# Performance work log

Measured on AMD Instinct MI355X. Metric: run time of the kernel, lower is better.

## Reference

```python
import jax, jax.numpy as jnp
import numpy as np


def setup_inputs() -> dict:
    key = jax.random.key(0)
    k1, k2 = jax.random.split(key)
    B, D, N = 4096, 3072, 50000  # chunk size, flattened CIFAR image dim, dataset size
    x = jax.random.normal(k1, (B, D), dtype=jnp.float32)
    y = jax.random.normal(k2, (B, D), dtype=jnp.float32)
    # buffers: initialized to +inf-like large value / zeros as in the torch module
    min_dists = jnp.full((N,), 1e9, dtype=jnp.float32)
    nn_indices = jnp.zeros((N,), dtype=jnp.int32)
    return {
        "x": x,
        "y": y,
        "min_dists": min_dists,
        "nn_indices": nn_indices,
        "x_idx_start": 1024,
        "y_idx_start": 4096,
    }


def reference(x, y, min_dists, nn_indices, x_idx_start, y_idx_start):
    # K == 1, cosine_dist == False path of KNNComputerNoCheck.forward
    B = x.shape[0]
    xf = x.reshape(B, -1)
    yf = y.reshape(y.shape[0], -1)
    # pairwise euclidean distances (same math as torch.cdist p=2)
    x2 = jnp.sum(xf * xf, axis=1, keepdims=True)        # [B,1]
    y2 = jnp.sum(yf * yf, axis=1)                        # [B]
    d2 = x2 + y2[None, :] - 2.0 * (xf @ yf.T)            # [B,B]
    dist = jnp.sqrt(jnp.maximum(d2, 0.0))
    new_min = jnp.min(dist, axis=1)                      # [B]
    nn = jnp.argmin(dist, axis=1).astype(nn_indices.dtype)
    # buffer scatter-update: min with existing slice, unconditional index overwrite
    old = jax.lax.dynamic_slice(min_dists, (x_idx_start,), (B,))
    min_dists = jax.lax.dynamic_update_slice(
        min_dists, jnp.minimum(new_min, old), (x_idx_start,))
    nn_indices = jax.lax.dynamic_update_slice(
        nn_indices, nn + jnp.int32(y_idx_start), (x_idx_start,))
    return min_dists, nn_indices
```

## Files before the change

### kernel.cpp

```cpp
#include <hip/hip_runtime.h>
#include <math.h>

#define BSZ 4096
#define DDIM 3072
#define QBM 256
#define QBN 256
#define QBK 64
#define NBUF 4
#define NT   (DDIM / QBK)
#define BM 128
#define BN 128
#define BK 32
#define LDK 40
#define S_Q 20.0f
#define DELTA 32.0f
#define NSLOT 16

typedef _Float16 half8 __attribute__((ext_vector_type(8)));
typedef float    floatx4 __attribute__((ext_vector_type(4)));
typedef int      intx4  __attribute__((ext_vector_type(4)));
typedef unsigned char u8;

__device__ __forceinline__ unsigned long long pack_key(float t, unsigned int j) {
    unsigned int b = __float_as_uint(t);
    b = (b & 0x80000000u) ? ~b : (b | 0x80000000u);
    return ((unsigned long long)b << 32) | (unsigned long long)j;
}

__device__ __forceinline__ float unpack_val(unsigned long long key) {
    unsigned int ub = (unsigned int)(key >> 32);
    unsigned int b = (ub & 0x80000000u) ? (ub ^ 0x80000000u) : ~ub;
    return __uint_as_float(b);
}

__device__ __forceinline__ void split_f16(float v, _Float16& hi, _Float16& lo) {
    hi = (_Float16)v;
    lo = (_Float16)(v - (float)hi);
}

__device__ __forceinline__ void gll16(const void* g, void* l) {
    __builtin_amdgcn_global_load_lds(
        (const __attribute__((address_space(1))) void*)g,
        (__attribute__((address_space(3))) void*)l,
        16, 0, 0);
}

__global__ __launch_bounds__(256)
void split_norms_kernel(const float* __restrict__ x, const float* __restrict__ y,
                        const float* __restrict__ mind_in, const int* __restrict__ nn_in,
                        const int* __restrict__ xs_p,
                        u8* __restrict__ A8, u8* __restrict__ B8,
                        float* __restrict__ x2, float* __restrict__ y2,
                        float* __restrict__ out_mind, float* __restrict__ out_nn,
                        int N) {
    {
        const int xs = *xs_p;
        const int n = blockIdx.x * 256 + threadIdx.x;
        if (n < N) {
            const int i = n - xs;
            if (i < 0 || i >= BSZ) {
                out_mind[n] = mind_in[n];
                out_nn[n]   = (float)nn_in[n];
            }
        }
    }

    const int lane = threadIdx.x & 63;
    const int row  = blockIdx.x * 4 + (threadIdx.x >> 6);
    const bool isx = row < BSZ;
    const int r = isx ? row : row - BSZ;
    const float* src = (isx ? x : y) + (size_t)r * DDIM;
    unsigned int* dst = (unsigned int*)((isx ? A8 : B8) + (size_t)r * DDIM);

    float s = 0.f;
    #pragma unroll
    for (int it = 0; it < 12; ++it) {
        float4 v = *(const float4*)(src + it * 256 + lane * 4);
        float fv[4] = {v.x, v.y, v.z, v.w};
        union { signed char b[4]; unsigned int u; } q;
        #pragma unroll
        for (int i = 0; i < 4; i++) {
            s += fv[i] * fv[i];
            int qi = __float2int_rn(fv[i] * S_Q);
            qi = (qi > 127) ? 127 : ((qi < -127) ? -127 : qi);
            q.b[i] = (signed char)qi;
        }
        dst[it * 64 + lane] = q.u;
    }
    #pragma unroll
    for (int off = 32; off > 0; off >>= 1) s += __shfl_down(s, off, 64);
    if (lane == 0) { if (isx) x2[r] = s; else y2[r] = s; }
}

__global__ __launch_bounds__(512, 1)
void gemm_i8_kernel(const u8* __restrict__ A8, const u8* __restrict__ B8,
                    const float* __restrict__ y2, _Float16* __restrict__ Dt) {
    extern __shared__ u8 smem[];
    u8* const sA = smem;
    u8* const sB = smem + NBUF * QBM * QBK;

    const int tid = threadIdx.x;
    const int bid = blockIdx.x;
    const int sw  = ((bid & 7) << 5) | (bid >> 3);
    const int row0 = (sw >> 4) * QBM;
    const int col0 = (sw & 15) * QBN;

    const int wid    = tid >> 6;
    const int lane   = tid & 63;
    const int wave_m = wid >> 2;
    const int wave_n = wid & 3;
    const int lrow   = lane & 15;
    const int quad   = lane >> 4;

    intx4 acc[8][4];
    #pragma unroll
    for (int m = 0; m < 8; m++)
        #pragma unroll
        for (int n = 0; n < 4; n++) acc[m][n] = (intx4){0, 0, 0, 0};

    const int rg = lane >> 2, cg = lane & 3;
    const int g  = cg ^ ((rg >> 1) & 3);
    const int wr = (wid & 3) * 64;
    const u8* stSrc = ((wid < 4) ? (A8 + (size_t)row0 * DDIM)
                                 : (B8 + (size_t)col0 * DDIM))
                      + (size_t)(wr + rg) * DDIM + g * 16;
    u8* stDst = ((wid < 4) ? sA : sB) + wr * QBK + lane * 16;

    const int coff = (quad ^ ((lrow >> 1) & 3)) * 16;

#define STAGE(T)                                                              \
    do {                                                                      \
        const u8* p_ = stSrc + (size_t)(T) * QBK;                             \
        u8* d_ = stDst + ((T) & 3) * (QBM * QBK);                             \
        _Pragma("unroll")                                                     \
        for (int it_ = 0; it_ < 4; ++it_)                                     \
            gll16(p_ + (size_t)16 * it_ * DDIM, d_ + it_ * 16 * QBK);         \
    } while (0)

#define READF(FA, FB, T)                                                      \
    do {                                                                      \
        const u8* bA_ = sA + ((T) & 3) * (QBM * QBK);                         \
        const u8* bB_ = sB + ((T) & 3) * (QBN * QBK);                         \
        _Pragma("unroll")                                                     \
        for (int m = 0; m < 8; m++)                                           \
            FA[m] = *(const intx4*)&bA_[(wave_m * 128 + m * 16 + lrow) * QBK + coff]; \
        _Pragma("unroll")                                                     \
        for (int n = 0; n < 4; n++)                                           \
            FB[n] = *(const intx4*)&bB_[(wave_n * 64 + n * 16 + lrow) * QBK + coff]; \
    } while (0)

#define MFMA_ALL(FA, FB)                                                      \
    do {                                                                      \
        __builtin_amdgcn_s_setprio(1);                                        \
        _Pragma("unroll")                                                     \
        for (int m = 0; m < 8; m++)                                           \
            _Pragma("unroll")                                                 \
            for (int n = 0; n < 4; n++)                                       \
                acc[m][n] = __builtin_amdgcn_mfma_i32_16x16x64_i8(            \
                    FA[m], FB[n], acc[m][n], 0, 0, 0);                        \
        __builtin_amdgcn_s_setprio(0);                                        \
    } while (0)

#define GSTEP(T, VM, CFA, CFB, NFA, NFB)                                      \
    do {                                                                      \
        asm volatile("s_waitcnt lgkmcnt(0)" ::: "memory");                    \
        asm volatile("s_waitcnt vmcnt(" VM ")" ::: "memory");                 \
        __builtin_amdgcn_s_barrier();                                         \
        __builtin_amdgcn_sched_barrier(0);                                    \
        if ((T) + 1 < NT) READF(NFA, NFB, (T) + 1);                           \
        if ((T) + 4 < NT) STAGE((T) + 4);                                     \
        MFMA_ALL(CFA, CFB);                                                   \
    } while (0)

    intx4 fa0[8], fb0[4], fa1[8], fb1[4];

    STAGE(0); STAGE(1); STAGE(2); STAGE(3);
    asm volatile("s_waitcnt vmcnt(12)" ::: "memory");
    __builtin_amdgcn_s_barrier();
    __builtin_amdgcn_sched_barrier(0);
    READF(fa0, fb0, 0);

    for (int t = 0; t < NT - 4; t += 2) {
        GSTEP(t,     "8", fa0, fb0, fa1, fb1);
        GSTEP(t + 1, "8", fa1, fb1, fa0, fb0);
    }
    GSTEP(NT - 4, "8", fa0, fb0, fa1, fb1);
    GSTEP(NT - 3, "4", fa1, fb1, fa0, fb0);
    GSTEP(NT - 2, "0", fa0, fb0, fa1, fb1);
    asm volatile("s_waitcnt lgkmcnt(0)" ::: "memory");
    MFMA_ALL(fa1, fb1);
#undef GSTEP
#undef MFMA_ALL
#undef READF
#undef STAGE

    const float inv2 = 2.0f / (S_Q * S_Q);
    float y2v[4];
    int   jv[4];
    #pragma unroll
    for (int n = 0; n < 4; n++) {
        jv[n]  = col0 + wave_n * 64 + n * 16 + lrow;
        y2v[n] = y2[jv[n]] - 3072.0f;
    }
    #pragma unroll
    for (int m = 0; m < 8; m++) {
        #pragma unroll
        for (int reg = 0; reg < 4; reg++) {
            const int i = row0 + wave_m * 128 + m * 16 + quad * 4 + reg;
            #pragma unroll
            for (int n = 0; n < 4; n++) {
                const float t = y2v[n] - inv2 * (float)acc[m][n][reg];
                Dt[(size_t)i * BSZ + jv[n]] = (_Float16)t;
            }
        }
    }
}

__global__ __launch_bounds__(256)
void scan_exact_kernel(const _Float16* __restrict__ Dt,
                       const float* __restrict__ x, const float* __restrict__ y,
                       const float* __restrict__ y2, const float* __restrict__ x2,
                       const float* __restrict__ mind_in,
                       const int* __restrict__ xs_p, const int* __restrict__ ys_p,
                       float* __restrict__ out_mind, float* __restrict__ out_nn) {
    const int lane = threadIdx.x & 63;
    const int wv   = threadIdx.x >> 6;
    const int row  = blockIdx.x * 4 + wv;
    const _Float16* p = Dt + (size_t)row * BSZ;

    __shared__ unsigned int cand[4][NSLOT];
    if (lane < NSLOT) cand[wv][lane] = 0u;

    float m = 1e30f;
    #pragma unroll
    for (int it = 0; it < 8; ++it) {
        half8 v = *(const half8*)(p + it * 512 + lane * 8);
        float lm = fminf(fminf(fminf((float)v[0], (float)v[1]),
                               fminf((float)v[2], (float)v[3])),
                         fminf(fminf((float)v[4], (float)v[5]),
                               fminf((float)v[6], (float)v[7])));
        m = fminf(m, lm);
    }
    #pragma unroll
    for (int off = 32; off > 0; off >>= 1) m = fminf(m, __shfl_xor(m, off, 64));
    const float thr = m + DELTA;

    unsigned int cnt = 0;
    const unsigned long long lanemask = (1ull << lane) - 1ull;
    #pragma unroll
    for (int it = 0; it < 8; ++it) {
        half8 v = *(const half8*)(p + it * 512 + lane * 8);
        #pragma unroll
        for (int j = 0; j < 8; ++j) {
            const bool ok = ((float)v[j] <= thr);
            const unsigned long long mk = __ballot(ok);
            if (ok) {
                const unsigned int pos = cnt + (unsigned int)__popcll(mk & lanemask);
                if (pos < NSLOT) cand[wv][pos] = it * 512 + lane * 8 + j;
            }
            cnt += (unsigned int)__popcll(mk);
        }
    }
    int cnum = (int)((cnt < NSLOT) ? cnt : NSLOT);

    const float* xr = x + (size_t)row * DDIM;
    float bt = 1e30f;
    int   bj = 0x7fffffff;
    for (int c = 0; c < cnum; ++c) {
        const int col = (int)(cand[wv][c] & (BSZ - 1));
        const float* yr = y + (size_t)col * DDIM;
        float s = 0.f;
        #pragma unroll
        for (int k = 0; k < 12; k++) {
            float4 a = *(const float4*)(xr + k * 256 + lane * 4);
            float4 b = *(const float4*)(yr + k * 256 + lane * 4);
            s += a.x * b.x + a.y * b.y + a.z * b.z + a.w * b.w;
        }
        #pragma unroll
        for (int off = 32; off > 0; off >>= 1) s += __shfl_down(s, off, 64);
        s = __shfl(s, 0, 64);
        const float t = y2[col] - 2.0f * s;
        if (t < bt || (t == bt && col < bj)) { bt = t; bj = col; }
    }

    if (lane == 0) {
        const int xs = *xs_p, ys = *ys_p;
        const int n = xs + row;
        const float d = sqrtf(fmaxf(x2[row] + bt, 0.f));
        out_mind[n] = fminf(mind_in[n], d);
        out_nn[n]   = (float)(bj + ys);
    }
}

__global__ __launch_bounds__(256)
void norms_init_kernel(const float* __restrict__ x, const float* __restrict__ y,
                       float* __restrict__ x2, float* __restrict__ y2,
                       unsigned long long* __restrict__ keys) {
    const int row = blockIdx.x;
    const float* p = (row < BSZ) ? (x + (size_t)row * DDIM)
                                 : (y + (size_t)(row - BSZ) * DDIM);
    const float4* p4 = (const float4*)p;
    float s = 0.f;
    for (int k = threadIdx.x; k < DDIM / 4; k += 256) {
        float4 v = p4[k];
        s += v.x * v.x + v.y * v.y + v.z * v.z + v.w * v.w;
    }
    #pragma unroll
    for (int off = 32; off > 0; off >>= 1) s += __shfl_down(s, off, 64);
    __shared__ float ls[4];
    const int lane = threadIdx.x & 63, w = threadIdx.x >> 6;
    if (lane == 0) ls[w] = s;
    __syncthreads();
    if (threadIdx.x == 0) {
        float tot = ls[0] + ls[1] + ls[2] + ls[3];
        if (row < BSZ) { x2[row] = tot; keys[row] = ~0ull; }
        else           { y2[row - BSZ] = tot; }
    }
}

__global__ __launch_bounds__(256, 3)
void gemm_min_kernel(const float* __restrict__ x, const float* __restrict__ y,
                     const float* __restrict__ y2,
                     unsigned long long* __restrict__ keys) {
    __shared__ _Float16 Ahi[BM * LDK];
    __shared__ _Float16 Alo[BM * LDK];
    __shared__ _Float16 Bhi[BN * LDK];
    __shared__ _Float16 Blo[BN * LDK];
    __shared__ unsigned long long rowmin[BM];

    const int tid  = threadIdx.x;
    const int row0 = blockIdx.y * BM;
    const int col0 = blockIdx.x * BN;
    const int wid    = tid >> 6;
    const int lane   = tid & 63;
    const int wave_m = wid & 1;
    const int wave_n = wid >> 1;
    const int lrow   = lane & 15;
    const int quad   = lane >> 4;

    floatx4 acc[4][4];
    #pragma unroll
    for (int m = 0; m < 4; m++)
        #pragma unroll
        for (int n = 0; n < 4; n++) acc[m][n] = (floatx4){0.f, 0.f, 0.f, 0.f};

    if (tid < BM) rowmin[tid] = ~0ull;

    const int sr = tid >> 1;
    const int sh = tid & 1;
    const float* Asrc = x + (size_t)(row0 + sr) * DDIM + sh * 16;
    const float* Bsrc = y + (size_t)(col0 + sr) * DDIM + sh * 16;
    _Float16* AhiW = &Ahi[sr * LDK + sh * 16];
    _Float16* AloW = &Alo[sr * LDK + sh * 16];
    _Float16* BhiW = &Bhi[sr * LDK + sh * 16];
    _Float16* BloW = &Blo[sr * LDK + sh * 16];

    for (int k0 = 0; k0 < DDIM; k0 += BK) {
        {
            float4 a0 = *(const float4*)(Asrc + k0 + 0);
            float4 a1 = *(const float4*)(Asrc + k0 + 4);
            float4 a2 = *(const float4*)(Asrc + k0 + 8);
            float4 a3 = *(const float4*)(Asrc + k0 + 12);
            float4 b0 = *(const float4*)(Bsrc + k0 + 0);
            float4 b1 = *(const float4*)(Bsrc + k0 + 4);
            float4 b2 = *(const float4*)(Bsrc + k0 + 8);
            float4 b3 = *(const float4*)(Bsrc + k0 + 12);
            float av[16] = {a0.x,a0.y,a0.z,a0.w, a1.x,a1.y,a1.z,a1.w,
                            a2.x,a2.y,a2.z,a2.w, a3.x,a3.y,a3.z,a3.w};
            float bv[16] = {b0.x,b0.y,b0.z,b0.w, b1.x,b1.y,b1.z,b1.w,
                            b2.x,b2.y,b2.z,b2.w, b3.x,b3.y,b3.z,b3.w};
            half8 ah0, ah1, al0, al1, bh0, bh1, bl0, bl1;
            #pragma unroll
            for (int i = 0; i < 8; i++) {
                _Float16 hi, lo;
                split_f16(av[i], hi, lo);     ah0[i] = hi; al0[i] = lo;
                split_f16(av[i + 8], hi, lo); ah1[i] = hi; al1[i] = lo;
                split_f16(bv[i], hi, lo);     bh0[i] = hi; bl0[i] = lo;
                split_f16(bv[i + 8], hi, lo); bh1[i] = hi; bl1[i] = lo;
            }
            __syncthreads();
            *(half8*)(AhiW + 0) = ah0;  *(half8*)(AhiW + 8) = ah1;
            *(half8*)(AloW + 0) = al0;  *(half8*)(AloW + 8) = al1;
            *(half8*)(BhiW + 0) = bh0;  *(half8*)(BhiW + 8) = bh1;
            *(half8*)(BloW + 0) = bl0;  *(half8*)(BloW + 8) = bl1;
        }
        __syncthreads();

        half8 fah[4], fal[4], fbh[4], fbl[4];
        #pragma unroll
        for (int m = 0; m < 4; m++) {
            const int r = wave_m * 64 + m * 16 + lrow;
            fah[m] = *(const half8*)&Ahi[r * LDK + quad * 8];
            fal[m] = *(const half8*)&Alo[r * LDK + quad * 8];
        }
        #pragma unroll
        for (int n = 0; n < 4; n++) {
            const int c = wave_n * 64 + n * 16 + lrow;
            fbh[n] = *(const half8*)&Bhi[c * LDK + quad * 8];
            fbl[n] = *(const half8*)&Blo[c * LDK + quad * 8];
        }
        #pragma unroll
        for (int m = 0; m < 4; m++)
            #pragma unroll
            for (int n = 0; n < 4; n++) {
                acc[m][n] = __builtin_amdgcn_mfma_f32_16x16x32_f16(fah[m], fbh[n], acc[m][n], 0, 0, 0);
                acc[m][n] = __builtin_amdgcn_mfma_f32_16x16x32_f16(fah[m], fbl[n], acc[m][n], 0, 0, 0);
                acc[m][n] = __builtin_amdgcn_mfma_f32_16x16x32_f16(fal[m], fbh[n], acc[m][n], 0, 0, 0);
            }
    }
    __syncthreads();

    float y2v[4];
    int   jv[4];
    #pragma unroll
    for (int n = 0; n < 4; n++) {
        jv[n]  = col0 + wave_n * 64 + n * 16 + lrow;
        y2v[n] = y2[jv[n]];
    }
    #pragma unroll
    for (int m = 0; m < 4; m++) {
        const int ibase = wave_m * 64 + m * 16 + quad * 4;
        #pragma unroll
        for (int reg = 0; reg < 4; reg++) {
            unsigned long long best = ~0ull;
            #pragma unroll
            for (int n = 0; n < 4; n++) {
                const float t = y2v[n] - 2.0f * acc[m][n][reg];
                const unsigned long long key = pack_key(t, (unsigned int)jv[n]);
                best = (key < best) ? key : best;
            }
            atomicMin(&rowmin[ibase + reg], best);
        }
    }
    __syncthreads();
    if (tid < BM) atomicMin(&keys[row0 + tid], rowmin[tid]);
}

__global__ __launch_bounds__(256)
void finalize_kernel(const float* __restrict__ mind_in, const int* __restrict__ nn_in,
                     const int* __restrict__ xs_p, const int* __restrict__ ys_p,
                     const unsigned long long* __restrict__ keys,
                     const float* __restrict__ x2,
                     float* __restrict__ out_mind, float* __restrict__ out_nn, int N) {
    const int n = blockIdx.x * blockDim.x + threadIdx.x;
    if (n >= N) return;
    const int xs = *xs_p, ys = *ys_p;
    float md  = mind_in[n];
    float nnv = (float)nn_in[n];
    const int i = n - xs;
    if (i >= 0 && i < BSZ) {
        const unsigned long long key = keys[i];
        const float t  = unpack_val(key);
        const float d2 = x2[i] + t;
        const float d  = sqrtf(fmaxf(d2, 0.f));
        md  = fminf(md, d);
        nnv = (float)((int)(key & 0xFFFFFFFFull) + ys);
    }
    out_mind[n] = md;
    out_nn[n]  = nnv;
}

extern "C" void kernel_launch(void* const* d_in, const int* in_sizes, int n_in,
                              void* d_out, int out_size, void* d_ws, size_t ws_size,
                              hipStream_t stream) {
    const float* x       = (const float*)d_in[0];
    const float* y       = (const float*)d_in[1];
    const float* mind_in = (const float*)d_in[2];
    const int*   nn_in   = (const int*)d_in[3];
    const int*   xs_p    = (const int*)d_in[4];
    const int*   ys_p    = (const int*)d_in[5];
    const int N = in_sizes[2];

    unsigned long long* keys = (unsigned long long*)d_ws;
    float* x2 = (float*)((char*)d_ws + 32768);
    float* y2 = (float*)((char*)d_ws + 49152);
    const size_t q_bytes = (size_t)BSZ * DDIM;
    u8* A8 = (u8*)((char*)d_ws + 344064);
    u8* B8 = A8 + q_bytes;
    _Float16* Dt = (_Float16*)(B8 + q_bytes);
    const size_t ws_needed = 344064 + 2 * q_bytes + (size_t)BSZ * BSZ * 2;

    float* out_mind = (float*)d_out;
    float* out_nn   = out_mind + N;

    if (ws_size >= ws_needed) {
        static bool s_attr_done = false;
        if (!s_attr_done) {
            (void)hipFuncSetAttribute((const void*)gemm_i8_kernel,
                                      hipFuncAttributeMaxDynamicSharedMemorySize,
                                      NBUF * (QBM + QBN) * QBK);
            s_attr_done = true;
        }
        split_norms_kernel<<<2 * BSZ / 4, 256, 0, stream>>>(
            x, y, mind_in, nn_in, xs_p, A8, B8, x2, y2, out_mind, out_nn, N);
        gemm_i8_kernel<<<(BSZ / QBM) * (BSZ / QBN), 512,
                         NBUF * (QBM + QBN) * QBK, stream>>>(A8, B8, y2, Dt);
        scan_exact_kernel<<<BSZ / 4, 256, 0, stream>>>(
            Dt, x, y, y2, x2, mind_in, xs_p, ys_p, out_mind, out_nn);
    } else {
        dim3 grid(BSZ / BN, BSZ / BM);
        norms_init_kernel<<<2 * BSZ, 256, 0, stream>>>(x, y, x2, y2, keys);
        gemm_min_kernel<<<grid, 256, 0, stream>>>(x, y, y2, keys);
        finalize_kernel<<<(N + 255) / 256, 256, 0, stream>>>(
            mind_in, nn_in, xs_p, ys_p, keys, x2, out_mind, out_nn, N);
    }
}
```

Before: 201.6 us.

## Split int8 GEMM k-step into four interleaved phases with single fragment buffer

Restructures the int8 MFMA main loop so that each k-tile runs in four phases. Each phase reads part of the A/B fragments from LDS, issues one global-to-LDS chunk for a tile three ahead, and runs 8 MFMAs. Register double-buffering of fragments is dropped in favour of a single buffer, and prefetch depth goes from four tiles to three. The goal is finer interleaving of LDS reads, global loads and MFMAs with lower register pressure, at the cost of more barriers per tile and a shallower prefetch.

Measured after the change: 207.7 us. +3.0%, slower.

```diff
diff --git a/kernel.cpp b/kernel.cpp
--- a/kernel.cpp
+++ b/kernel.cpp
@@ -118,6 +118,8 @@
         #pragma unroll
         for (int n = 0; n < 4; n++) acc[m][n] = (intx4){0, 0, 0, 0};
 
+    intx4 fa[8], fb[4];
+
     const int rg = lane >> 2, cg = lane & 3;
     const int g  = cg ^ ((rg >> 1) & 3);
     const int wr = (wid & 3) * 64;
@@ -128,71 +130,75 @@
 
     const int coff = (quad ^ ((lrow >> 1) & 3)) * 16;
 
-#define STAGE(T)                                                              \
+#define STAGE_CHUNK(T, C)                                                     \
     do {                                                                      \
-        const u8* p_ = stSrc + (size_t)(T) * QBK;                             \
-        u8* d_ = stDst + ((T) & 3) * (QBM * QBK);                             \
+        if ((T) < NT) {                                                       \
+            gll16(stSrc + (size_t)(T) * QBK + (size_t)16 * (C) * DDIM,        \
+                  stDst + ((T) & 3) * (QBM * QBK) + (C) * 16 * QBK);          \
+        }                                                                     \
+    } while (0)
+
+#define RD_FA(M) fa[M] = *(const intx4*)&bA[(wave_m * 128 + (M) * 16 + lrow) * QBK + coff]
+#define RD_FB(Nn) fb[Nn] = *(const intx4*)&bB[(wave_n * 64 + (Nn) * 16 + lrow) * QBK + coff]
+
+#define MFMA8(MM0, NN0)                                                       \
+    _Pragma("unroll")                                                         \
+    for (int m_ = 0; m_ < 4; m_++)                                            \
         _Pragma("unroll")                                                     \
-        for (int it_ = 0; it_ < 4; ++it_)                                     \
-            gll16(p_ + (size_t)16 * it_ * DDIM, d_ + it_ * 16 * QBK);         \
-    } while (0)
-
-#define READF(FA, FB, T)                                                      \
+        for (int n_ = 0; n_ < 2; n_++)                                        \
+            acc[(MM0) + m_][(NN0) + n_] = __builtin_amdgcn_mfma_i32_16x16x64_i8( \
+                fa[(MM0) + m_], fb[(NN0) + n_], acc[(MM0) + m_][(NN0) + n_], 0, 0, 0)
+
+#define PHASE_TAIL(T, CH, MM0, NN0)                                           \
+    STAGE_CHUNK((T) + 3, CH);                                                 \
+    __builtin_amdgcn_s_barrier();                                             \
+    asm volatile("s_waitcnt lgkmcnt(0)" ::: "memory");                        \
+    __builtin_amdgcn_sched_barrier(0);                                        \
+    __builtin_amdgcn_s_setprio(1);                                            \
+    MFMA8(MM0, NN0);                                                          \
+    __builtin_amdgcn_s_setprio(0)
+
+#define TILE(T, VM)                                                           \
     do {                                                                      \
-        const u8* bA_ = sA + ((T) & 3) * (QBM * QBK);                         \
-        const u8* bB_ = sB + ((T) & 3) * (QBN * QBK);                         \
-        _Pragma("unroll")                                                     \
-        for (int m = 0; m < 8; m++)                                           \
-            FA[m] = *(const intx4*)&bA_[(wave_m * 128 + m * 16 + lrow) * QBK + coff]; \
-        _Pragma("unroll")                                                     \
-        for (int n = 0; n < 4; n++)                                           \
-            FB[n] = *(const intx4*)&bB_[(wave_n * 64 + n * 16 + lrow) * QBK + coff]; \
-    } while (0)
-
-#define MFMA_ALL(FA, FB)                                                      \
-    do {                                                                      \
-        __builtin_amdgcn_s_setprio(1);                                        \
-        _Pragma("unroll")                                                     \
-        for (int m = 0; m < 8; m++)                                           \
-            _Pragma("unroll")                                                 \
-            for (int n = 0; n < 4; n++)                                       \
-                acc[m][n] = __builtin_amdgcn_mfma_i32_16x16x64_i8(            \
-                    FA[m], FB[n], acc[m][n], 0, 0, 0);                        \
-        __builtin_amdgcn_s_setprio(0);                                        \
-    } while (0)
-
-#define GSTEP(T, VM, CFA, CFB, NFA, NFB)                                      \
-    do {                                                                      \
-        asm volatile("s_waitcnt lgkmcnt(0)" ::: "memory");                    \
+        const u8* bA = sA + ((T) & 3) * (QBM * QBK);                          \
+        const u8* bB = sB + ((T) & 3) * (QBN * QBK);                          \
+                                                                 \
+        RD_FA(0); RD_FA(1); RD_FA(2); RD_FA(3); RD_FB(0); RD_FB(1);           \
+        PHASE_TAIL(T, 0, 0, 0);                                               \
+        __builtin_amdgcn_s_barrier();                                         \
+                                                                 \
+        RD_FB(2); RD_FB(3);                                                   \
+        PHASE_TAIL(T, 1, 0, 2);                                               \
+        __builtin_amdgcn_s_barrier();                                         \
+                                                                 \
+        RD_FA(4); RD_FA(5); RD_FA(6); RD_FA(7);                               \
+        PHASE_TAIL(T, 2, 4, 0);                                               \
+        __builtin_amdgcn_s_barrier();                                         \
+                                                      \
+        PHASE_TAIL(T, 3, 4, 2);                                               \
         asm volatile("s_waitcnt vmcnt(" VM ")" ::: "memory");                 \
         __builtin_amdgcn_s_barrier();                                         \
-        __builtin_amdgcn_sched_barrier(0);                                    \
-        if ((T) + 1 < NT) READF(NFA, NFB, (T) + 1);                           \
-        if ((T) + 4 < NT) STAGE((T) + 4);                                     \
-        MFMA_ALL(CFA, CFB);                                                   \
     } while (0)
 
-    intx4 fa0[8], fb0[4], fa1[8], fb1[4];
-
-    STAGE(0); STAGE(1); STAGE(2); STAGE(3);
-    asm volatile("s_waitcnt vmcnt(12)" ::: "memory");
+    #pragma unroll
+    for (int tt = 0; tt < 3; ++tt) {
+        STAGE_CHUNK(tt, 0); STAGE_CHUNK(tt, 1);
+        STAGE_CHUNK(tt, 2); STAGE_CHUNK(tt, 3);
+    }
+    asm volatile("s_waitcnt vmcnt(8)" ::: "memory");
     __builtin_amdgcn_s_barrier();
     __builtin_amdgcn_sched_barrier(0);
-    READF(fa0, fb0, 0);
-
-    for (int t = 0; t < NT - 4; t += 2) {
-        GSTEP(t,     "8", fa0, fb0, fa1, fb1);
-        GSTEP(t + 1, "8", fa1, fb1, fa0, fb0);
-    }
-    GSTEP(NT - 4, "8", fa0, fb0, fa1, fb1);
-    GSTEP(NT - 3, "4", fa1, fb1, fa0, fb0);
-    GSTEP(NT - 2, "0", fa0, fb0, fa1, fb1);
-    asm volatile("s_waitcnt lgkmcnt(0)" ::: "memory");
-    MFMA_ALL(fa1, fb1);
-#undef GSTEP
-#undef MFMA_ALL
-#undef READF
-#undef STAGE
+
+    for (int t = 0; t < NT - 3; ++t) TILE(t, "8");
+    TILE(NT - 3, "4");
+    TILE(NT - 2, "0");
+    TILE(NT - 1, "0");
+#undef TILE
+#undef PHASE_TAIL
+#undef MFMA8
+#undef RD_FB
+#undef RD_FA
+#undef STAGE_CHUNK
 
     const float inv2 = 2.0f / (S_Q * S_Q);
     float y2v[4];
```
